# Kernel tuning notes

Hardware: AMD Instinct MI355X
Metric: run time of the kernel (lower is better)

Reference implementation:

```python
import jax, jax.numpy as jnp
import numpy as np

NEG_INF = -9e15  # matches torch's -9000000000000000.0 mask value
ALPHA = 0.2      # LeakyReLU negative slope


def setup_inputs() -> dict:
    key = jax.random.key(0)
    k1, k2, k3, k4 = jax.random.split(key, 4)
    B, N, Fin, Fout = 8, 2048, 256, 256
    h = jax.random.normal(k1, (B, N, Fin), dtype=jnp.float32)
    adj = jax.random.randint(k2, (B, N, N), 0, 2, dtype=jnp.int32)
    # xavier_uniform with gain=1.414
    limW = 1.414 * np.sqrt(6.0 / (Fin + Fout))
    W = jax.random.uniform(k3, (Fin, Fout), minval=-limW, maxval=limW, dtype=jnp.float32)
    lima = 1.414 * np.sqrt(6.0 / (2 * Fout + 1))
    a = jax.random.uniform(k4, (2 * Fout, 1), minval=-lima, maxval=lima, dtype=jnp.float32)
    return {"h": h, "adj": adj, "W": W, "a": a}


def reference(h, adj, W, a):
    # h: (B, N, Fin), adj: (B, N, N), W: (Fin, Fout), a: (2*Fout, 1)
    Fout = W.shape[1]
    Wh = jnp.einsum('bni,io->bno', h, W)                 # (B, N, Fout)
    # e[b,i,j] = leakyrelu(Wh[b,i] @ a1 + Wh[b,j] @ a2) -- equivalent to the
    # original concat([Wh_i, Wh_j]) @ a without the O(N^2 * 2F) intermediate.
    e1 = Wh @ a[:Fout, 0]                                # (B, N)
    e2 = Wh @ a[Fout:, 0]                                # (B, N)
    e = jax.nn.leaky_relu(e1[:, :, None] + e2[:, None, :], negative_slope=ALPHA)
    masked = jnp.where(adj > 0, e, NEG_INF)
    attention = jax.nn.softmax(masked, axis=-1)          # (B, N, N)
    # dropout omitted (deterministic eval-mode reference)
    h_prime = jnp.einsum('bij,bjo->bio', attention, Wh)  # (B, N, Fout)
    return jax.nn.elu(h_prime), attention
```

## Files before the change

kernel.cpp:

```cpp
#include <hip/hip_runtime.h>
#include <hip/hip_bf16.h>
#include <stdint.h>

#define NEG_INF -9.0e15f
#define LRELU_ALPHA 0.2f
#define LOG2E 1.442695040888963f

using bf16x8  = __attribute__((ext_vector_type(8))) short;
using f32x4   = __attribute__((ext_vector_type(4))) float;
using short4v = __attribute__((ext_vector_type(4))) short;
using int4v   = __attribute__((ext_vector_type(4))) int;
using float4v = __attribute__((ext_vector_type(4))) float;
using uint2v  = __attribute__((ext_vector_type(2))) unsigned;
using uint4v  = __attribute__((ext_vector_type(4))) unsigned;

static __device__ __forceinline__ short f2bf(float f) {
  unsigned u = __builtin_bit_cast(unsigned, f);
  u = u + 0x7FFFu + ((u >> 16) & 1u);
  return (short)(u >> 16);
}
static __device__ __forceinline__ unsigned cvtpk_bf16(float lo, float hi) {
  unsigned r;
  asm volatile("v_cvt_pk_bf16_f32 %0, %1, %2" : "=v"(r) : "v"(lo), "v"(hi));
  return r;
}
static __device__ __forceinline__ void gload16(const void* g, void* l) {
  __builtin_amdgcn_global_load_lds((const __attribute__((address_space(1))) void*)g,
                                   (__attribute__((address_space(3))) void*)l, 16, 0, 0);
}

__global__ __launch_bounds__(256) void prep_kernel(
    const float* __restrict__ W, const float* __restrict__ a,
    short* __restrict__ W_t, float* __restrict__ aW1, float* __restrict__ aW2)
{
  const int bid = blockIdx.x;
  const int tid = threadIdx.x;
  if (bid < 16) {
    __shared__ float t[64][65];
    const int m0 = (bid & 3) * 64, n0 = (bid >> 2) * 64;
    const int rr = tid >> 3, cc = (tid & 7) * 8;
#pragma unroll
    for (int p = 0; p < 2; ++p) {
      int row = rr + p * 32;
      const float* sp = W + (m0 + row) * 256 + n0 + cc;
      float4v v0 = *(const float4v*)sp;
      float4v v1 = *(const float4v*)(sp + 4);
#pragma unroll
      for (int j = 0; j < 4; ++j) { t[row][cc + j] = v0[j]; t[row][cc + 4 + j] = v1[j]; }
    }
    __syncthreads();
#pragma unroll
    for (int p = 0; p < 2; ++p) {
      int orow = rr + p * 32;
      short vv[8] __attribute__((aligned(16)));
#pragma unroll
      for (int j = 0; j < 8; ++j) vv[j] = f2bf(t[cc + j][orow]);
      short* dp = W_t + (n0 + orow) * 256 + m0 + cc;
      *(int4v*)dp = *(const int4v*)vv;
    }
  } else {
    const int r8 = tid >> 3, o4 = (tid & 7) * 4;
    float s1[8] = {}, s2[8] = {};
#pragma unroll
    for (int rp = 0; rp < 8; ++rp) {
      int row = r8 + rp * 32;
#pragma unroll
      for (int k = 0; k < 8; ++k) {
        int o = o4 + k * 32;
        float4v wv = *(const float4v*)(W + row * 256 + o);
        float4v a1 = *(const float4v*)(a + o);
        float4v a2 = *(const float4v*)(a + 256 + o);
#pragma unroll
        for (int e = 0; e < 4; ++e) { s1[rp] += wv[e] * a1[e]; s2[rp] += wv[e] * a2[e]; }
      }
    }
#pragma unroll
    for (int rp = 0; rp < 8; ++rp) {
#pragma unroll
      for (int off = 4; off > 0; off >>= 1) {
        s1[rp] += __shfl_xor(s1[rp], off, 64);
        s2[rp] += __shfl_xor(s2[rp], off, 64);
      }
      if ((tid & 7) == 0) { aW1[r8 + rp * 32] = s1[rp]; aW2[r8 + rp * 32] = s2[rp]; }
    }
  }
}

__global__ __launch_bounds__(256) void gemm_h_kernel(
    const float* __restrict__ A, const short* __restrict__ Bt,
    short* __restrict__ Wht, const float* __restrict__ aW1,
    const float* __restrict__ aW2, float* __restrict__ e1, float* __restrict__ e2)
{
  __shared__ short As[128 * 32];
  __shared__ short Bs[128 * 32];
  __shared__ short T[128][136];
  const int m0 = blockIdx.x * 128, n0 = blockIdx.y * 128;
  const int tid = threadIdx.x;
  const int w = tid >> 6, lane = tid & 63;
  const int wr = w >> 1, wc = w & 1;
  const int g = lane >> 4, lr = lane & 15;
  const bool doE = (blockIdx.y == 0);

  f32x4 acc[4][4] = {};
  float s1q[2] = {0.f, 0.f}, s2q[2] = {0.f, 0.f};

  for (int k0 = 0; k0 < 256; k0 += 32) {
    __syncthreads();
#pragma unroll
    for (int q = 0; q < 2; ++q) {
      int c = q * 256 + tid;
      int row = c >> 2, kq = (c & 3) << 3;
      const float* ap = A + (long long)(m0 + row) * 256 + k0 + kq;
      float4v u0 = *(const float4v*)ap;
      float4v u1 = *(const float4v*)(ap + 4);
      if (doE) {
        float4v w1a = *(const float4v*)(aW1 + k0 + kq);
        float4v w1b = *(const float4v*)(aW1 + k0 + kq + 4);
        float4v w2a = *(const float4v*)(aW2 + k0 + kq);
        float4v w2b = *(const float4v*)(aW2 + k0 + kq + 4);
#pragma unroll
        for (int e = 0; e < 4; ++e) {
          s1q[q] += u0[e] * w1a[e] + u1[e] * w1b[e];
          s2q[q] += u0[e] * w2a[e] + u1[e] * w2b[e];
        }
      }
      uint4v uv;
      uv[0] = cvtpk_bf16(u0[0], u0[1]);
      uv[1] = cvtpk_bf16(u0[2], u0[3]);
      uv[2] = cvtpk_bf16(u1[0], u1[1]);
      uv[3] = cvtpk_bf16(u1[2], u1[3]);
      *(bf16x8*)(As + c * 8) = __builtin_bit_cast(bf16x8, uv);
    }
#pragma unroll
    for (int q = 0; q < 2; ++q) {
      int p = w * 2 + q;
      int c = p * 64 + lane;
      int row = c >> 2, kq = (c & 3) << 3;
      gload16(Bt + (long long)(n0 + row) * 256 + k0 + kq, Bs + p * 512);
    }
    __syncthreads();

    bf16x8 af[4], bfr[4];
#pragma unroll
    for (int i = 0; i < 4; ++i) {
      af[i]  = *(const bf16x8*)(As + (wr * 64 + i * 16 + lr) * 32 + 8 * g);
      bfr[i] = *(const bf16x8*)(Bs + (wc * 64 + i * 16 + lr) * 32 + 8 * g);
    }
#pragma unroll
    for (int i = 0; i < 4; ++i)
#pragma unroll
      for (int j = 0; j < 4; ++j)
        acc[i][j] = __builtin_amdgcn_mfma_f32_16x16x32_bf16(af[i], bfr[j], acc[i][j], 0, 0, 0);
  }

  if (doE) {
#pragma unroll
    for (int q = 0; q < 2; ++q) {
      float a1 = s1q[q], a2 = s2q[q];
      a1 += __shfl_xor(a1, 1, 64); a1 += __shfl_xor(a1, 2, 64);
      a2 += __shfl_xor(a2, 1, 64); a2 += __shfl_xor(a2, 2, 64);
      if ((tid & 3) == 0) {
        int row = m0 + q * 64 + (tid >> 2);
        e1[row] = a1; e2[row] = a2;
      }
    }
  }

  __syncthreads();
#pragma unroll
  for (int i = 0; i < 4; ++i) {
    int row_base = wr * 64 + i * 16 + 4 * g;
#pragma unroll
    for (int j = 0; j < 4; ++j) {
      int col = wc * 64 + j * 16 + lr;
#pragma unroll
      for (int r = 0; r < 4; ++r)
        T[col][row_base + r] = f2bf(acc[i][j][r]);
    }
  }
  __syncthreads();
  const int b = m0 >> 11, mloc = m0 & 2047;
  short* wb = Wht + (long long)b * 524288 + mloc;
#pragma unroll
  for (int p = 0; p < 8; ++p) {
    int c = (tid >> 4) + p * 16;
    int off = (tid & 15) * 8;
    bf16x8 v = *(const bf16x8*)(&T[c][off]);
    *(bf16x8*)(wb + (long long)(n0 + c) * 2048 + off) = v;
  }
}

__global__ __launch_bounds__(256) void attn_softmax_kernel(
    const int* __restrict__ adj, const float* __restrict__ e1,
    const float* __restrict__ e2, float* __restrict__ attn)
{
  const int i = blockIdx.x;
  const int b = blockIdx.y;
  const long long row = (long long)b * 2048 + i;
  const int tid = threadIdx.x;
  const int wid = tid >> 6, lane = tid & 63;
  const int j0 = tid * 8;

  const int*   arow = adj + row * 2048 + j0;
  const float  ei   = e1[row];
  const float* e2b  = e2 + b * 2048 + j0;

  int4v   a0 = *(const int4v*)(arow);
  int4v   a1 = *(const int4v*)(arow + 4);
  float4v f0 = *(const float4v*)(e2b);
  float4v f1 = *(const float4v*)(e2b + 4);

  float s[8];
#pragma unroll
  for (int k = 0; k < 8; ++k) {
    float x = ei + (k < 4 ? f0[k] : f1[k - 4]);
    float v = x > 0.f ? x : LRELU_ALPHA * x;
    int  ad = (k < 4 ? a0[k] : a1[k - 4]);
    s[k] = (ad > 0) ? v : NEG_INF;
  }
  float m = s[0];
#pragma unroll
  for (int k = 1; k < 8; ++k) m = fmaxf(m, s[k]);
#pragma unroll
  for (int off = 32; off > 0; off >>= 1) m = fmaxf(m, __shfl_xor(m, off, 64));

  __shared__ float wmax[4], wsum[4];
  if (lane == 0) wmax[wid] = m;
  __syncthreads();
  const float M = fmaxf(fmaxf(wmax[0], wmax[1]), fmaxf(wmax[2], wmax[3]));

  float p[8]; float t = 0.f;
#pragma unroll
  for (int k = 0; k < 8; ++k) { p[k] = __expf(s[k] - M); t += p[k]; }
#pragma unroll
  for (int off = 32; off > 0; off >>= 1) t += __shfl_xor(t, off, 64);
  if (lane == 0) wsum[wid] = t;
  __syncthreads();
  const float S = wsum[0] + wsum[1] + wsum[2] + wsum[3];
  const float r = 1.0f / S;

  float4v o0, o1;
#pragma unroll
  for (int k = 0; k < 4; ++k) { o0[k] = p[k] * r; o1[k] = p[k + 4] * r; }
  float* op = attn + row * 2048 + j0;
  *(float4v*)op       = o0;
  *(float4v*)(op + 4) = o1;
}

__global__ __launch_bounds__(256, 3) void pv_kernel(
    const float* __restrict__ attn, const short* __restrict__ Bt, float* __restrict__ C)
{
  __shared__ float As0[32 * 32], As1[32 * 32];
  __shared__ short Bs0[256 * 32], Bs1[256 * 32];
  const int bid = blockIdx.x;
  const int bz  = bid & 7;
  const int M0  = (bid >> 3) << 5;
  const int tid = threadIdx.x;
  const int w = tid >> 6, lane = tid & 63;
  const int g = lane >> 4, lr = lane & 15;

  attn += (long long)bz * 4194304;
  Bt   += (long long)bz * 524288;
  C    += (long long)bz * 524288;

  const int a_s  = w * 64 + lane;
  const int a_r  = a_s >> 3, a_cs = a_s & 7;
  const int a_dc = a_cs ^ (a_r & 7);
  const float* aSrc = attn + (long long)(M0 + a_r) * 2048 + a_dc * 4;

  const int bcol_off = lane >> 2;
  const int bchunk   = (lane & 3) ^ ((lane >> 3) & 3);

  f32x4 acc[2][4] = {};

  auto STAGE = [&](short* BsD, float* AsD, int k0) {
#pragma unroll
    for (int q = 0; q < 4; ++q) {
      int pp = w * 4 + q;
      int col = pp * 16 + bcol_off;
      gload16(Bt + (long long)col * 2048 + k0 + bchunk * 8, BsD + pp * 512);
    }
    gload16(aSrc + k0, (char*)AsD + w * 1024);
  };

  auto COMPUTE = [&](const short* BsD, const float* AsD) {
    bf16x8 af[2], bfr[4];
#pragma unroll
    for (int i = 0; i < 2; ++i) {
      int row = i * 16 + lr;
      const float* ar = AsD + row * 32;
      float4v lo = *(const float4v*)(ar + (((2 * g)     ^ (row & 7)) << 2));
      float4v hi = *(const float4v*)(ar + (((2 * g + 1) ^ (row & 7)) << 2));
      uint4v uv;
      uv[0] = cvtpk_bf16(lo[0], lo[1]);
      uv[1] = cvtpk_bf16(lo[2], lo[3]);
      uv[2] = cvtpk_bf16(hi[0], hi[1]);
      uv[3] = cvtpk_bf16(hi[2], hi[3]);
      af[i] = __builtin_bit_cast(bf16x8, uv);
    }
#pragma unroll
    for (int j = 0; j < 4; ++j) {
      int col = w * 64 + j * 16 + lr;
      bfr[j] = *(const bf16x8*)(BsD + col * 32 + ((g ^ ((col >> 1) & 3)) << 3));
    }
#pragma unroll
    for (int i = 0; i < 2; ++i)
#pragma unroll
      for (int j = 0; j < 4; ++j)
        acc[i][j] = __builtin_amdgcn_mfma_f32_16x16x32_bf16(af[i], bfr[j], acc[i][j], 0, 0, 0);
  };

  STAGE(Bs0, As0, 0);
  __syncthreads();
  for (int t = 0; t < 64; t += 2) {
    STAGE(Bs1, As1, (t + 1) * 32);
    COMPUTE(Bs0, As0);
    __syncthreads();
    if (t + 2 < 64) STAGE(Bs0, As0, (t + 2) * 32);
    COMPUTE(Bs1, As1);
    __syncthreads();
  }

#pragma unroll
  for (int i = 0; i < 2; ++i) {
    int row_base = M0 + i * 16 + 4 * g;
#pragma unroll
    for (int j = 0; j < 4; ++j) {
      int col = w * 64 + j * 16 + lr;
#pragma unroll
      for (int r = 0; r < 4; ++r) {
        float v = acc[i][j][r];
        v = (v > 0.f) ? v : (__expf(v) - 1.f);
        C[(long long)(row_base + r) * 256 + col] = v;
      }
    }
  }
}

extern "C" void kernel_launch(void* const* d_in, const int* in_sizes, int n_in,
                              void* d_out, int out_size, void* d_ws, size_t ws_size,
                              hipStream_t stream)
{
  const float* h   = (const float*)d_in[0];
  const int*   adj = (const int*)d_in[1];
  const float* W   = (const float*)d_in[2];
  const float* a   = (const float*)d_in[3];

  float* hp_out   = (float*)d_out;
  float* attn_out = hp_out + 4194304LL;

  short* W_t  = (short*)d_ws;
  short* Wh_t = W_t + 65536;
  float* e1   = (float*)(Wh_t + 4194304);
  float* e2   = e1 + 16384;
  float* aW1  = e2 + 16384;
  float* aW2  = aW1 + 256;

  prep_kernel<<<17, 256, 0, stream>>>(W, a, W_t, aW1, aW2);
  gemm_h_kernel<<<dim3(128, 2), 256, 0, stream>>>(h, W_t, Wh_t, aW1, aW2, e1, e2);
  attn_softmax_kernel<<<dim3(2048, 8), 256, 0, stream>>>(adj, e1, e2, attn_out);
  pv_kernel<<<512, 256, 0, stream>>>(attn_out, Wh_t, hp_out);
}
```

Before: 121.6 us.

## Replace double-buffered PV GEMM with single-buffered 64-wide K tiles and register-converted A

The attention-times-Wh GEMM drops the double-buffered async global-to-LDS pipeline for a single-buffered loop with K tiles of 64 instead of 32. The fp32 attention tile is now loaded into registers, converted to bf16 once, and stored to LDS, so the inner loop reads bf16 A fragments directly. Occupancy is raised to four blocks per SM. The cost is losing overlap between loads and MFMA work, since each iteration waits on synchronous A loads between two barriers.

```diff
diff --git a/kernel.cpp b/kernel.cpp
--- a/kernel.cpp
+++ b/kernel.cpp
@@ -4,14 +4,12 @@
 
 #define NEG_INF -9.0e15f
 #define LRELU_ALPHA 0.2f
-#define LOG2E 1.442695040888963f
 
 using bf16x8  = __attribute__((ext_vector_type(8))) short;
 using f32x4   = __attribute__((ext_vector_type(4))) float;
 using short4v = __attribute__((ext_vector_type(4))) short;
 using int4v   = __attribute__((ext_vector_type(4))) int;
 using float4v = __attribute__((ext_vector_type(4))) float;
-using uint2v  = __attribute__((ext_vector_type(2))) unsigned;
 using uint4v  = __attribute__((ext_vector_type(4))) unsigned;
 
 static __device__ __forceinline__ short f2bf(float f) {
@@ -247,83 +245,77 @@
   *(float4v*)(op + 4) = o1;
 }
 
-__global__ __launch_bounds__(256, 3) void pv_kernel(
-    const float* __restrict__ attn, const short* __restrict__ Bt, float* __restrict__ C)
-{
-  __shared__ float As0[32 * 32], As1[32 * 32];
-  __shared__ short Bs0[256 * 32], Bs1[256 * 32];
+__global__ __launch_bounds__(256, 4) void gemm_attn_kernel(
+    const float* __restrict__ A, const short* __restrict__ Bt,
+    float* __restrict__ C)
+{
+  __shared__ short As[32 * 64];
+  __shared__ short Bs[256 * 64];
   const int bid = blockIdx.x;
-  const int bz  = bid & 7;
-  const int M0  = (bid >> 3) << 5;
+  const int bz = bid & 7;
+  const int m0 = (bid >> 3) << 5;
+  A  += (long long)bz * 4194304;
+  Bt += (long long)bz * 524288;
+  C  += (long long)bz * 524288;
   const int tid = threadIdx.x;
   const int w = tid >> 6, lane = tid & 63;
   const int g = lane >> 4, lr = lane & 15;
 
-  attn += (long long)bz * 4194304;
-  Bt   += (long long)bz * 524288;
-  C    += (long long)bz * 524288;
-
-  const int a_s  = w * 64 + lane;
-  const int a_r  = a_s >> 3, a_cs = a_s & 7;
-  const int a_dc = a_cs ^ (a_r & 7);
-  const float* aSrc = attn + (long long)(M0 + a_r) * 2048 + a_dc * 4;
-
-  const int bcol_off = lane >> 2;
-  const int bchunk   = (lane & 3) ^ ((lane >> 3) & 3);
-
   f32x4 acc[2][4] = {};
 
-  auto STAGE = [&](short* BsD, float* AsD, int k0) {
-#pragma unroll
-    for (int q = 0; q < 4; ++q) {
-      int pp = w * 4 + q;
-      int col = pp * 16 + bcol_off;
-      gload16(Bt + (long long)col * 2048 + k0 + bchunk * 8, BsD + pp * 512);
-    }
-    gload16(aSrc + k0, (char*)AsD + w * 1024);
-  };
-
-  auto COMPUTE = [&](const short* BsD, const float* AsD) {
-    bf16x8 af[2], bfr[4];
+  const int ar = tid >> 3, ac8 = tid & 7;
+  short* as_wr = As + ar * 64 + ((ac8 ^ (ar & 7)) << 3);
+  const float* a_rd_base = A + (long long)(m0 + ar) * 2048 + ac8 * 8;
+
+  const int bcol_off = lane >> 3;
+  const int bchunk   = (lane & 7) ^ ((lane >> 3) & 7);
+
+  for (int k0 = 0; k0 < 2048; k0 += 64) {
+    __syncthreads();
+    {
+      const float* ap = a_rd_base + k0;
+      float4v u0 = *(const float4v*)ap;
+      float4v u1 = *(const float4v*)(ap + 4);
+      short os[8] __attribute__((aligned(16)));
+#pragma unroll
+      for (int k = 0; k < 8; ++k) os[k] = f2bf(k < 4 ? u0[k] : u1[k - 4]);
+      *(bf16x8*)as_wr = *(const bf16x8*)os;
+    }
+#pragma unroll
+    for (int q = 0; q < 8; ++q) {
+      int p = w * 8 + q;
+      int col = p * 8 + bcol_off;
+      gload16(Bt + (long long)col * 2048 + k0 + bchunk * 8, Bs + p * 512);
+    }
+    __syncthreads();
+
+    bf16x8 af[2][2], bfr[4][2];
 #pragma unroll
     for (int i = 0; i < 2; ++i) {
       int row = i * 16 + lr;
-      const float* ar = AsD + row * 32;
-      float4v lo = *(const float4v*)(ar + (((2 * g)     ^ (row & 7)) << 2));
-      float4v hi = *(const float4v*)(ar + (((2 * g + 1) ^ (row & 7)) << 2));
-      uint4v uv;
-      uv[0] = cvtpk_bf16(lo[0], lo[1]);
-      uv[1] = cvtpk_bf16(lo[2], lo[3]);
-      uv[2] = cvtpk_bf16(hi[0], hi[1]);
-      uv[3] = cvtpk_bf16(hi[2], hi[3]);
-      af[i] = __builtin_bit_cast(bf16x8, uv);
+#pragma unroll
+      for (int s = 0; s < 2; ++s)
+        af[i][s] = *(const bf16x8*)(As + row * 64 + (((s * 4 + g) ^ (row & 7)) << 3));
     }
 #pragma unroll
     for (int j = 0; j < 4; ++j) {
       int col = w * 64 + j * 16 + lr;
-      bfr[j] = *(const bf16x8*)(BsD + col * 32 + ((g ^ ((col >> 1) & 3)) << 3));
-    }
-#pragma unroll
-    for (int i = 0; i < 2; ++i)
-#pragma unroll
-      for (int j = 0; j < 4; ++j)
-        acc[i][j] = __builtin_amdgcn_mfma_f32_16x16x32_bf16(af[i], bfr[j], acc[i][j], 0, 0, 0);
-  };
-
-  STAGE(Bs0, As0, 0);
-  __syncthreads();
-  for (int t = 0; t < 64; t += 2) {
-    STAGE(Bs1, As1, (t + 1) * 32);
-    COMPUTE(Bs0, As0);
-    __syncthreads();
-    if (t + 2 < 64) STAGE(Bs0, As0, (t + 2) * 32);
-    COMPUTE(Bs1, As1);
-    __syncthreads();
+#pragma unroll
+      for (int s = 0; s < 2; ++s)
+        bfr[j][s] = *(const bf16x8*)(Bs + col * 64 + (((s * 4 + g) ^ (col & 7)) << 3));
+    }
+#pragma unroll
+    for (int s = 0; s < 2; ++s)
+#pragma unroll
+      for (int i = 0; i < 2; ++i)
+#pragma unroll
+        for (int j = 0; j < 4; ++j)
+          acc[i][j] = __builtin_amdgcn_mfma_f32_16x16x32_bf16(af[i][s], bfr[j][s], acc[i][j], 0, 0, 0);
   }
 
 #pragma unroll
   for (int i = 0; i < 2; ++i) {
-    int row_base = M0 + i * 16 + 4 * g;
+    int row_base = m0 + i * 16 + 4 * g;
 #pragma unroll
     for (int j = 0; j < 4; ++j) {
       int col = w * 64 + j * 16 + lr;
@@ -359,5 +351,5 @@
   prep_kernel<<<17, 256, 0, stream>>>(W, a, W_t, aW1, aW2);
   gemm_h_kernel<<<dim3(128, 2), 256, 0, stream>>>(h, W_t, Wh_t, aW1, aW2, e1, e2);
   attn_softmax_kernel<<<dim3(2048, 8), 256, 0, stream>>>(adj, e1, e2, attn_out);
-  pv_kernel<<<512, 256, 0, stream>>>(attn_out, Wh_t, hp_out);
-}
+  gemm_attn_kernel<<<512, 256, 0, stream>>>(attn_out, Wh_t, hp_out);
+}
```

Measured after the change: 113.9 us. -6.3%, faster.
